# Kernel tuning notes

Hardware: AMD Instinct MI355X
Metric: run time of the kernel (lower is better)

Reference implementation:

```python
import jax, jax.numpy as jnp
import numpy as np

B, S, D = 4, 4096, 2048  # batch, seq, hidden
E, R, K = 8, 16, 2       # n_experts, rank, top_k


def setup_inputs() -> dict:
    key = jax.random.key(0)
    k1, k2, k3, k4 = jax.random.split(key, 4)
    x = jax.random.normal(k1, (B, S, D), dtype=jnp.float32)
    router_w = jax.random.normal(k2, (E, D), dtype=jnp.float32) * 0.02  # nn.Linear weight (out,in)
    experts_down = jax.random.normal(k3, (E, D, R), dtype=jnp.float32) * 0.01
    experts_up = jax.random.normal(k4, (E, R, D), dtype=jnp.float32) * 0.01
    return {"x": x, "router_w": router_w, "experts_down": experts_down, "experts_up": experts_up}


def reference(x, router_w, experts_down, experts_up):
    E_ = router_w.shape[0]
    # router sees detached x (torch: self.router(x.detach()))
    logits = jnp.einsum('bsd,ed->bse', jax.lax.stop_gradient(x), router_w)
    w, idx = jax.lax.top_k(logits, K)          # (B,S,K)
    w = jax.nn.softmax(w, axis=-1)
    # combined per-token, per-expert routing weight; zero for non-selected experts
    w_full = jnp.sum(jax.nn.one_hot(idx, E_, dtype=x.dtype) * w[..., None], axis=2)  # (B,S,E)
    # rank-space activations per expert: (B,S,E,R) -- small (R=16)
    h = jnp.einsum('bsd,edr->bser', x, experts_down)
    # fuse routing weight into rank space, then up-project and sum over experts
    out = x + jnp.einsum('bser,bse,erd->bsd', h, w_full, experts_up)
    return out
```

## Files before the change

kernel.cpp:

```cpp
#include <hip/hip_runtime.h>
#include <hip/hip_bf16.h>

#define MTOK 16384
#define DDIM 2048
#define NEXP 8
#define RNK 16
#define NC 128
#define NW 160
#define LOGIT0 128
#define KSPLIT 2
#define KLEN (DDIM / KSPLIT)
#define NT (KLEN / 64)

typedef __attribute__((ext_vector_type(8))) short bf16x8;
typedef __attribute__((ext_vector_type(4))) short short4v;
typedef __attribute__((ext_vector_type(4))) float f32x4;

typedef __attribute__((address_space(1))) const void gv_t;
typedef __attribute__((address_space(3))) void lv_t;

__device__ __forceinline__ short f2b(float f) {
  unsigned u = __float_as_uint(f);
  u += 0x7fffu + ((u >> 16) & 1u);
  return (short)(u >> 16);
}
__device__ __forceinline__ float b2f(short s) {
  return __uint_as_float(((unsigned)(unsigned short)s) << 16);
}

__global__ __launch_bounds__(256) void prep_k(const float* __restrict__ rw,
                                              const float* __restrict__ down,
                                              const float* __restrict__ up,
                                              short* __restrict__ WdT,
                                              short* __restrict__ UT) {
  int i = blockIdx.x * 256 + threadIdx.x;
  const int NWD = NW * DDIM;
  const int NUT = DDIM * NC;
  if (i < NWD) {
    int n = i / DDIM, k = i % DDIM;
    int s = (k >> 3) & 7;
    int src_k = (k & ~0x3F) | ((s ^ (n & 7)) << 3) | (k & 7);
    float v = 0.f;
    if (n < NC)             v = down[((n >> 4) * DDIM + src_k) * RNK + (n & 15)];
    else if (n < NC + NEXP) v = rw[(n - NC) * DDIM + src_k];
    WdT[i] = f2b(v);
  } else if (i < NWD + NUT) {
    int u = i - NWD;
    int c = u >> 7, j = u & 127;
    UT[u] = f2b(up[((j >> 4) * RNK + (j & 15)) * DDIM + c]);
  }
}

__global__ __launch_bounds__(256, 4) void gemm1_k(const float* __restrict__ X,
                                                  const short* __restrict__ WdT,
                                                  short* __restrict__ Hp) {
  __shared__ short Al[2][64][72];
  __shared__ short Bl[2][160 * 64];
  const int tid = threadIdx.x;
  const int lane = tid & 63;
  const int w = tid >> 6;
  const int gm0 = blockIdx.x * 64;
  const int ks = blockIdx.y;
  const int kb = ks * KLEN;
  const int wr = (w & 1) * 32;
  const int wc = (w >> 1) * 80;
  const int lr = lane & 15;
  const int lk = (lane >> 4) * 8;

  f32x4 acc[2][5];
#pragma unroll
  for (int m = 0; m < 2; ++m)
#pragma unroll
    for (int n = 0; n < 5; ++n) acc[m][n] = (f32x4){0.f, 0.f, 0.f, 0.f};

  float4 aR[2][4];

  auto loadA = [&](int k0, int s) {
#pragma unroll
    for (int i2 = 0; i2 < 4; ++i2) {
      int f = tid + 256 * i2;
      int row = f >> 4, c4 = f & 15;
      aR[s][i2] = *(const float4*)(X + (size_t)(gm0 + row) * DDIM + k0 + c4 * 4);
    }
  };
  auto issueB = [&](int buf, int k0) {
#pragma unroll
    for (int j = 0; j < 5; ++j) {
      int u = (w * 5 + j) * 64 + lane;
      const short* g = WdT + (size_t)(u >> 3) * DDIM + k0 + (u & 7) * 8;
      short* l = &Bl[buf][(w * 5 + j) * 512];
      __builtin_amdgcn_global_load_lds((gv_t*)g, (lv_t*)l, 16, 0, 0);
    }
  };
  auto writeA = [&](int buf, int s) {
#pragma unroll
    for (int i2 = 0; i2 < 4; ++i2) {
      int f = tid + 256 * i2;
      int row = f >> 4, c4 = f & 15;
      short4v v;
      v.x = f2b(aR[s][i2].x); v.y = f2b(aR[s][i2].y);
      v.z = f2b(aR[s][i2].z); v.w = f2b(aR[s][i2].w);
      *(short4v*)&Al[buf][row][c4 * 4] = v;
    }
  };
  auto compute = [&](int buf) {
#pragma unroll
    for (int kk2 = 0; kk2 < 2; ++kk2) {
      const int kk = kk2 * 32;
      bf16x8 a[2], b[5];
#pragma unroll
      for (int m = 0; m < 2; ++m)
        a[m] = *(const bf16x8*)&Al[buf][wr + m * 16 + lr][kk + lk];
#pragma unroll
      for (int n = 0; n < 5; ++n) {
        int row = wc + n * 16 + lr;
        int sl = ((kk >> 3) + (lane >> 4)) ^ (row & 7);
        b[n] = *(const bf16x8*)&Bl[buf][row * 64 + sl * 8];
      }
#pragma unroll
      for (int m = 0; m < 2; ++m)
#pragma unroll
        for (int n = 0; n < 5; ++n)
          acc[m][n] = __builtin_amdgcn_mfma_f32_16x16x32_bf16(a[m], b[n], acc[m][n], 0, 0, 0);
    }
  };

  loadA(kb, 0);
  issueB(0, kb);
  loadA(kb + 64, 1);
  issueB(1, kb + 64);
  asm volatile("s_waitcnt vmcnt(12)" ::: "memory");
  __builtin_amdgcn_sched_barrier(0);
  writeA(0, 0);
  asm volatile("s_waitcnt vmcnt(7)" ::: "memory");
  asm volatile("s_waitcnt lgkmcnt(0)" ::: "memory");
  __builtin_amdgcn_sched_barrier(0);
  __builtin_amdgcn_s_barrier();

#pragma unroll
  for (int t = 0; t < NT; ++t) {
    if (t + 2 < NT) loadA(kb + (t + 2) * 64, t & 1);
    compute(t & 1);
    asm volatile("s_waitcnt lgkmcnt(0)" ::: "memory");
    __builtin_amdgcn_s_barrier();
    __builtin_amdgcn_sched_barrier(0);
    if (t + 2 < NT) issueB(t & 1, kb + (t + 2) * 64);
    if (t + 1 < NT) {
      if (t + 2 < NT)
        asm volatile("s_waitcnt vmcnt(7)" ::: "memory");
      else
        asm volatile("s_waitcnt vmcnt(0)" ::: "memory");
      __builtin_amdgcn_sched_barrier(0);
      writeA((t + 1) & 1, (t + 1) & 1);
      asm volatile("s_waitcnt lgkmcnt(0)" ::: "memory");
      __builtin_amdgcn_sched_barrier(0);
    }
    __builtin_amdgcn_s_barrier();
  }

  short* Hq = Hp + (size_t)ks * MTOK * NW;
  const int cr = (lane >> 4) * 4;
#pragma unroll
  for (int m = 0; m < 2; ++m)
#pragma unroll
    for (int n = 0; n < 5; ++n)
#pragma unroll
      for (int r = 0; r < 4; ++r) {
        int row = gm0 + wr + m * 16 + cr + r;
        int col = wc + n * 16 + lr;
        Hq[(size_t)row * NW + col] = f2b(acc[m][n][r]);
      }
}

__global__ __launch_bounds__(256) void gemm2_k(const short* __restrict__ Hp,
                                               const short* __restrict__ UT,
                                               const float* __restrict__ X,
                                               float* __restrict__ Out) {
  __shared__ short Al[128][136];
  __shared__ short Bl[64][136];
  const int tid = threadIdx.x;
  const int lane = tid & 63;
  const int w = tid >> 6;
  const int gm0 = blockIdx.x * 128;
  const int n0 = blockIdx.y * 64;
  const int lr = lane & 15;
  const int lk = (lane >> 4) * 8;
  const short* Hp1 = Hp + (size_t)MTOK * NW;

  float4 xPf[8];
#pragma unroll
  for (int j = 0; j < 8; ++j) {
    int c = lane + 64 * j;
    int rl = c >> 4, c4 = c & 15;
    xPf[j] = *(const float4*)(X + (size_t)(gm0 + w * 32 + rl) * DDIM + n0 + c4 * 4);
  }

  if (tid < 128) {
    int t = gm0 + tid;
    uint4 l0 = *(const uint4*)(Hp  + (size_t)t * NW + LOGIT0);
    uint4 l1 = *(const uint4*)(Hp1 + (size_t)t * NW + LOGIT0);
    const short* p0 = (const short*)&l0;
    const short* p1 = (const short*)&l1;
    float lgv[8];
#pragma unroll
    for (int e = 0; e < 8; ++e) lgv[e] = b2f(p0[e]) + b2f(p1[e]);
    float b0 = -1e30f, b1 = -1e30f;
    int i0 = 0, i1 = 0;
#pragma unroll
    for (int e = 0; e < 8; ++e) {
      float v = lgv[e];
      if (v > b0) { b1 = b0; i1 = i0; b0 = v; i0 = e; }
      else if (v > b1) { b1 = v; i1 = e; }
    }
    float ex = __expf(b1 - b0);
    float inv = 1.f / (1.f + ex);
#pragma unroll
    for (int e = 0; e < 8; ++e)
      Al[tid][128 + e] = f2b((e == i0) ? inv : ((e == i1) ? ex * inv : 0.f));
  }
#pragma unroll
  for (int i = 0; i < 4; ++i) {
    int f = tid + 256 * i;
    int row = f >> 4, c8 = f & 15;
    *(uint4*)&Bl[row][c8 * 8] = *(const uint4*)(UT + (size_t)(n0 + row) * NC + c8 * 8);
  }
  __syncthreads();

#pragma unroll
  for (int i = 0; i < 8; ++i) {
    int f = tid + 256 * i;
    int row = f >> 4, c8 = f & 15;
    uint4 h0 = *(const uint4*)(Hp  + (size_t)(gm0 + row) * NW + c8 * 8);
    uint4 h1 = *(const uint4*)(Hp1 + (size_t)(gm0 + row) * NW + c8 * 8);
    const short* p0 = (const short*)&h0;
    const short* p1 = (const short*)&h1;
    float wgt = b2f(Al[row][128 + (c8 >> 1)]);
    short r[8];
#pragma unroll
    for (int e = 0; e < 8; ++e)
      r[e] = f2b((b2f(p0[e]) + b2f(p1[e])) * wgt);
    *(uint4*)&Al[row][c8 * 8] = *(uint4*)r;
  }
  __syncthreads();

  f32x4 acc[2][4];
#pragma unroll
  for (int m = 0; m < 2; ++m)
#pragma unroll
    for (int n = 0; n < 4; ++n) acc[m][n] = (f32x4){0.f, 0.f, 0.f, 0.f};

#pragma unroll
  for (int ks = 0; ks < 4; ++ks) {
    const int kk = ks * 32;
    bf16x8 a[2], b[4];
#pragma unroll
    for (int m = 0; m < 2; ++m) a[m] = *(const bf16x8*)&Al[w * 32 + m * 16 + lr][kk + lk];
#pragma unroll
    for (int n = 0; n < 4; ++n) b[n] = *(const bf16x8*)&Bl[n * 16 + lr][kk + lk];
#pragma unroll
    for (int m = 0; m < 2; ++m)
#pragma unroll
      for (int n = 0; n < 4; ++n)
        acc[m][n] = __builtin_amdgcn_mfma_f32_16x16x32_bf16(a[m], b[n], acc[m][n], 0, 0, 0);
  }

  float* eps = (float*)&Al[0][0] + w * 2176;
  const int cr = (lane >> 4) * 4;
#pragma unroll
  for (int m = 0; m < 2; ++m)
#pragma unroll
    for (int n = 0; n < 4; ++n)
#pragma unroll
      for (int r = 0; r < 4; ++r)
        eps[(m * 16 + cr + r) * 68 + n * 16 + lr] = acc[m][n][r];

#pragma unroll
  for (int j = 0; j < 8; ++j) {
    int c = lane + 64 * j;
    int rl = c >> 4, c4 = c & 15;
    float4 v = *(const float4*)&eps[rl * 68 + c4 * 4];
    size_t idx = (size_t)(gm0 + w * 32 + rl) * DDIM + n0 + c4 * 4;
    v.x += xPf[j].x; v.y += xPf[j].y; v.z += xPf[j].z; v.w += xPf[j].w;
    *(float4*)(Out + idx) = v;
  }
}

extern "C" void kernel_launch(void* const* d_in, const int* in_sizes, int n_in,
                              void* d_out, int out_size, void* d_ws, size_t ws_size,
                              hipStream_t stream) {
  const float* x    = (const float*)d_in[0];
  const float* rw   = (const float*)d_in[1];
  const float* down = (const float*)d_in[2];
  const float* up   = (const float*)d_in[3];
  float* out = (float*)d_out;

  char* ws = (char*)d_ws;
  short* WdT = (short*)ws;
  short* UT  = (short*)(ws + 655360);
  short* Hp  = (short*)(ws + 1179648);

  prep_k<<<2304, 256, 0, stream>>>(rw, down, up, WdT, UT);
  gemm1_k<<<dim3(MTOK / 64, KSPLIT), 256, 0, stream>>>(x, WdT, Hp);
  gemm2_k<<<dim3(MTOK / 128, DDIM / 64), 256, 0, stream>>>(Hp, UT, x, out);
}
```

Baseline: 92.07 us.

## Reuse routed rank activations across eight N tiles per block in gemm2

The up-projection kernel now launches 512 persistent-style blocks, each building the weighted rank-space A tile once, holding it in registers, and looping over eight 64-column output tiles. This removes the repeated Hp loads, routing top-k and reweighting that were previously redone for every one of the 32 column blocks. Output stores become nontemporal. The trade-off is fewer blocks with a serial per-block loop, where the X prefetch is no longer issued ahead of the whole computation, plus extra barriers per iteration.

Result: faster. 81.95 us (median of 2 runs) (-11.0%).

```diff
diff --git a/kernel.cpp b/kernel.cpp
--- a/kernel.cpp
+++ b/kernel.cpp
@@ -172,28 +172,21 @@
       }
 }
 
-__global__ __launch_bounds__(256) void gemm2_k(const short* __restrict__ Hp,
-                                               const short* __restrict__ UT,
-                                               const float* __restrict__ X,
-                                               float* __restrict__ Out) {
-  __shared__ short Al[128][136];
+__global__ __launch_bounds__(256, 2) void gemm2m_k(const short* __restrict__ Hp,
+                                                   const short* __restrict__ UT,
+                                                   const float* __restrict__ X,
+                                                   float* __restrict__ Out) {
   __shared__ short Bl[64][136];
+  __shared__ short At[128][136];
   const int tid = threadIdx.x;
   const int lane = tid & 63;
   const int w = tid >> 6;
-  const int gm0 = blockIdx.x * 128;
-  const int n0 = blockIdx.y * 64;
+  const int mb = blockIdx.x & 127, q = blockIdx.x >> 7;
+  const int gm0 = mb * 128;
+  const int nbase = q * 512;
   const int lr = lane & 15;
   const int lk = (lane >> 4) * 8;
   const short* Hp1 = Hp + (size_t)MTOK * NW;
-
-  float4 xPf[8];
-#pragma unroll
-  for (int j = 0; j < 8; ++j) {
-    int c = lane + 64 * j;
-    int rl = c >> 4, c4 = c & 15;
-    xPf[j] = *(const float4*)(X + (size_t)(gm0 + w * 32 + rl) * DDIM + n0 + c4 * 4);
-  }
 
   if (tid < 128) {
     int t = gm0 + tid;
@@ -216,13 +209,7 @@
     float inv = 1.f / (1.f + ex);
 #pragma unroll
     for (int e = 0; e < 8; ++e)
-      Al[tid][128 + e] = f2b((e == i0) ? inv : ((e == i1) ? ex * inv : 0.f));
-  }
-#pragma unroll
-  for (int i = 0; i < 4; ++i) {
-    int f = tid + 256 * i;
-    int row = f >> 4, c8 = f & 15;
-    *(uint4*)&Bl[row][c8 * 8] = *(const uint4*)(UT + (size_t)(n0 + row) * NC + c8 * 8);
+      At[tid][128 + e] = f2b((e == i0) ? inv : ((e == i1) ? ex * inv : 0.f));
   }
   __syncthreads();
 
@@ -234,54 +221,78 @@
     uint4 h1 = *(const uint4*)(Hp1 + (size_t)(gm0 + row) * NW + c8 * 8);
     const short* p0 = (const short*)&h0;
     const short* p1 = (const short*)&h1;
-    float wgt = b2f(Al[row][128 + (c8 >> 1)]);
+    float wgt = b2f(At[row][128 + (c8 >> 1)]);
     short r[8];
 #pragma unroll
     for (int e = 0; e < 8; ++e)
       r[e] = f2b((b2f(p0[e]) + b2f(p1[e])) * wgt);
-    *(uint4*)&Al[row][c8 * 8] = *(uint4*)r;
+    *(uint4*)&At[row][c8 * 8] = *(uint4*)r;
   }
   __syncthreads();
 
-  f32x4 acc[2][4];
+  bf16x8 af[2][4];
 #pragma unroll
   for (int m = 0; m < 2; ++m)
 #pragma unroll
-    for (int n = 0; n < 4; ++n) acc[m][n] = (f32x4){0.f, 0.f, 0.f, 0.f};
-
-#pragma unroll
-  for (int ks = 0; ks < 4; ++ks) {
-    const int kk = ks * 32;
-    bf16x8 a[2], b[4];
-#pragma unroll
-    for (int m = 0; m < 2; ++m) a[m] = *(const bf16x8*)&Al[w * 32 + m * 16 + lr][kk + lk];
-#pragma unroll
-    for (int n = 0; n < 4; ++n) b[n] = *(const bf16x8*)&Bl[n * 16 + lr][kk + lk];
+    for (int kc = 0; kc < 4; ++kc)
+      af[m][kc] = *(const bf16x8*)&At[w * 32 + m * 16 + lr][kc * 32 + lk];
+  __syncthreads();
+
+  float* eps = (float*)&At[0][0] + w * 2176;
+  const int cr = (lane >> 4) * 4;
+
+#pragma unroll 1
+  for (int it = 0; it < 8; ++it) {
+    const int n0 = nbase + it * 64;
+    float4 xPf[8];
+#pragma unroll
+    for (int j = 0; j < 8; ++j) {
+      int c = lane + 64 * j;
+      int rl = c >> 4, c4 = c & 15;
+      xPf[j] = *(const float4*)(X + (size_t)(gm0 + w * 32 + rl) * DDIM + n0 + c4 * 4);
+    }
+#pragma unroll
+    for (int i = 0; i < 4; ++i) {
+      int f = tid + 256 * i;
+      int row = f >> 4, c8 = f & 15;
+      *(uint4*)&Bl[row][c8 * 8] = *(const uint4*)(UT + (size_t)(n0 + row) * NC + c8 * 8);
+    }
+    __syncthreads();
+
+    f32x4 acc[2][4];
 #pragma unroll
     for (int m = 0; m < 2; ++m)
 #pragma unroll
+      for (int n = 0; n < 4; ++n) acc[m][n] = (f32x4){0.f, 0.f, 0.f, 0.f};
+#pragma unroll
+    for (int kc = 0; kc < 4; ++kc) {
+      bf16x8 b[4];
+#pragma unroll
+      for (int n = 0; n < 4; ++n) b[n] = *(const bf16x8*)&Bl[n * 16 + lr][kc * 32 + lk];
+#pragma unroll
+      for (int m = 0; m < 2; ++m)
+#pragma unroll
+        for (int n = 0; n < 4; ++n)
+          acc[m][n] = __builtin_amdgcn_mfma_f32_16x16x32_bf16(af[m][kc], b[n], acc[m][n], 0, 0, 0);
+    }
+
+#pragma unroll
+    for (int m = 0; m < 2; ++m)
+#pragma unroll
       for (int n = 0; n < 4; ++n)
-        acc[m][n] = __builtin_amdgcn_mfma_f32_16x16x32_bf16(a[m], b[n], acc[m][n], 0, 0, 0);
-  }
-
-  float* eps = (float*)&Al[0][0] + w * 2176;
-  const int cr = (lane >> 4) * 4;
-#pragma unroll
-  for (int m = 0; m < 2; ++m)
-#pragma unroll
-    for (int n = 0; n < 4; ++n)
-#pragma unroll
-      for (int r = 0; r < 4; ++r)
-        eps[(m * 16 + cr + r) * 68 + n * 16 + lr] = acc[m][n][r];
-
-#pragma unroll
-  for (int j = 0; j < 8; ++j) {
-    int c = lane + 64 * j;
-    int rl = c >> 4, c4 = c & 15;
-    float4 v = *(const float4*)&eps[rl * 68 + c4 * 4];
-    size_t idx = (size_t)(gm0 + w * 32 + rl) * DDIM + n0 + c4 * 4;
-    v.x += xPf[j].x; v.y += xPf[j].y; v.z += xPf[j].z; v.w += xPf[j].w;
-    *(float4*)(Out + idx) = v;
+#pragma unroll
+        for (int r = 0; r < 4; ++r)
+          eps[(m * 16 + cr + r) * 68 + n * 16 + lr] = acc[m][n][r];
+#pragma unroll
+    for (int j = 0; j < 8; ++j) {
+      int c = lane + 64 * j;
+      int rl = c >> 4, c4 = c & 15;
+      f32x4 v = *(const f32x4*)&eps[rl * 68 + c4 * 4];
+      size_t idx = (size_t)(gm0 + w * 32 + rl) * DDIM + n0 + c4 * 4;
+      v[0] += xPf[j].x; v[1] += xPf[j].y; v[2] += xPf[j].z; v[3] += xPf[j].w;
+      __builtin_nontemporal_store(v, (f32x4*)(Out + idx));
+    }
+    __syncthreads();
   }
 }
 
@@ -301,5 +312,5 @@
 
   prep_k<<<2304, 256, 0, stream>>>(rw, down, up, WdT, UT);
   gemm1_k<<<dim3(MTOK / 64, KSPLIT), 256, 0, stream>>>(x, WdT, Hp);
-  gemm2_k<<<dim3(MTOK / 128, DDIM / 64), 256, 0, stream>>>(Hp, UT, x, out);
-}
+  gemm2m_k<<<512, 256, 0, stream>>>(Hp, UT, x, out);
+}
```
